# Optimization experiments

Hardware: AMD Instinct MI355X
Metric: run time of the kernel (lower is better)

The kernel has to match this reference:

```python
import jax, jax.numpy as jnp
import numpy as np

LN_EPS = 1e-5
DELTA_FACTOR = 0.01
PATCH_KH, PATCH_KW = 4, 4
SIGMA = 2.0


def layernorm(x, g, b):
    m = jnp.mean(x, axis=-1, keepdims=True)
    v = jnp.var(x, axis=-1, keepdims=True)
    return (x - m) * jax.lax.rsqrt(v + LN_EPS) * g + b


def grid_sample(src, grid):
    # src [B,C,H,W], grid [B,Hg,Wg,2] in [-1,1]; bilinear, align_corners=False, zero padding
    B, C, H, W = src.shape
    Hg, Wg = grid.shape[1], grid.shape[2]
    gx = (grid[..., 0] + 1.0) * (W * 0.5) - 0.5
    gy = (grid[..., 1] + 1.0) * (H * 0.5) - 0.5
    x0 = jnp.floor(gx)
    y0 = jnp.floor(gy)
    wx = gx - x0
    wy = gy - y0
    x0i = x0.astype(jnp.int32)
    y0i = y0.astype(jnp.int32)
    flat = src.reshape(B, C, H * W)

    def tap(xi, yi, w):
        valid = (xi >= 0) & (xi < W) & (yi >= 0) & (yi < H)
        idx = (jnp.clip(yi, 0, H - 1) * W + jnp.clip(xi, 0, W - 1)).reshape(B, -1)
        vals = jax.vmap(lambda f, i: f[:, i])(flat, idx)  # [B,C,Hg*Wg]
        return vals * (w * valid).reshape(B, 1, -1)

    out = (tap(x0i, y0i, (1 - wx) * (1 - wy)) + tap(x0i + 1, y0i, wx * (1 - wy))
           + tap(x0i, y0i + 1, (1 - wx) * wy) + tap(x0i + 1, y0i + 1, wx * wy))
    return out.reshape(B, C, Hg, Wg)


def gaussian_filt(x, k, sigma):
    # depthwise Gaussian blur, NCHW
    C = x.shape[1]
    coords = jnp.arange(k, dtype=x.dtype) - (k - 1) / 2.0
    g2 = jnp.exp(-(coords[:, None] ** 2 + coords[None, :] ** 2) / (2.0 * sigma ** 2))
    g2 = g2 / g2.sum()
    kern = jnp.broadcast_to(g2, (C, 1, k, k))
    p = (k - 1) // 2
    return jax.lax.conv_general_dilated(x, kern, (1, 1), [(p, p), (p, p)],
                                        dimension_numbers=('NCHW', 'OIHW', 'NCHW'),
                                        feature_group_count=C)


def reconstruct_feature(feature, mask, k, sigma):
    if k <= 1:
        return feature
    feature = feature * mask
    out = gaussian_filt(jnp.concatenate([feature, mask], axis=1), k, sigma)
    f_i = out[:, :-1]
    m_i = out[:, -1:]
    f_i = f_i / (m_i + 1e-6)
    f_i = f_i * (m_i > 0)
    return feature + (1 - mask) * f_i


def token2map(x, loc, H, W, k, sigma):
    B, N, C = x.shape
    l = jnp.clip(loc, 0.0, 1.0) * jnp.array([W - 1, H - 1], dtype=loc.dtype)
    l = jnp.round(l).astype(jnp.int32)
    idx = l[..., 0] + l[..., 1] * W + (jnp.arange(B, dtype=jnp.int32) * (H * W))[:, None]
    vals = jnp.concatenate([x, jnp.ones((B, N, 1), x.dtype)], axis=-1).reshape(B * N, C + 1)
    out = jnp.zeros((B * H * W, C + 1), x.dtype).at[idx.reshape(-1)].add(vals)
    out = out.reshape(B, H, W, C + 1).transpose(0, 3, 1, 2)
    feat, mask = out[:, :-1], out[:, -1:]
    feat = feat / (mask + 1e-6)
    mask = (mask > 0).astype(x.dtype)
    feat = feat * mask
    return reconstruct_feature(feat, mask, k, sigma)


def forward(x, loc, src, H, W, kernel_size,
            w_delta, b_delta, norm1_g, norm1_b, conv_w, conv_b,
            norm2_g, norm2_b, fc1_w, fc1_b, fc2_w, fc2_b):
    B, N, _ = loc.shape
    Cs, Hs, Ws = src.shape[1], src.shape[2], src.shape[3]
    delta = (layernorm(x, norm1_g, norm1_b) @ w_delta + b_delta) * DELTA_FACTOR
    loc_extra = jnp.clip(loc + delta, 0.0, 1.0)
    # extract_local_feature: 4x4 sub-pixel patch around each extra location
    xo = (jnp.arange(PATCH_KW, dtype=loc.dtype) - (PATCH_KW - 1) / 2.0) / (Ws - 1)
    yo = (jnp.arange(PATCH_KH, dtype=loc.dtype) - (PATCH_KH - 1) / 2.0) / (Hs - 1)
    off = jnp.stack([jnp.broadcast_to(xo[None, :], (PATCH_KH, PATCH_KW)),
                     jnp.broadcast_to(yo[:, None], (PATCH_KH, PATCH_KW))], axis=-1)
    grid = (loc_extra[:, :, None, None, :] + off[None, None]) * 2.0 - 1.0  # [B,N,kh,kw,2]
    patches = grid_sample(src, grid.reshape(B, N, PATCH_KH * PATCH_KW, 2))  # [B,C,N,kh*kw]
    patches = patches.reshape(B, Cs, N, PATCH_KH, PATCH_KW)
    # local_conv: 4x4 conv stride 4 over a 4x4 patch == single dot product
    extra = jnp.einsum('bcnhw,ochw->bno', patches, conv_w) + conv_b
    extra = layernorm(extra, norm2_g, norm2_b)
    # token2map scatter + gaussian reconstruction, then gather back at loc_extra
    fmap = token2map(x, loc, H, W, kernel_size, SIGMA)
    extra_inter = grid_sample(fmap, (loc_extra * 2.0 - 1.0)[:, None, :, :])  # [B,C,1,N]
    extra_inter = extra_inter[:, :, 0].transpose(0, 2, 1)  # [B,N,C]
    extra = jnp.concatenate([extra_inter, extra], axis=-1)
    h = jax.nn.gelu(extra @ fc1_w + fc1_b, approximate=False)
    extra = h @ fc2_w + fc2_b
    return jnp.concatenate([x, extra], axis=1), jnp.concatenate([loc, loc_extra], axis=1)


def setup_inputs() -> dict:
    key = jax.random.key(0)
    ks = jax.random.split(key, 12)
    B, N, D = 4, 16384, 256
    LD, HID = 64, 4 * D
    inp = {
        'x': jax.random.normal(ks[0], (B, N, D), jnp.float32),
        'loc': jax.random.uniform(ks[1], (B, N, 2), jnp.float32),
        'src': jax.random.normal(ks[2], (B, 3, 512, 512), jnp.float32),
        'pos_embed': jnp.zeros((1,), jnp.float32),
        'H': 128, 'W': 128, 'kernel_size': 3,
        'w_delta': jax.random.normal(ks[3], (D, 2), jnp.float32) * 0.02,
        'b_delta': jnp.zeros((2,), jnp.float32),
        'norm1_g': jnp.ones((D,), jnp.float32),
        'norm1_b': jnp.zeros((D,), jnp.float32),
        'conv_w': jax.random.normal(ks[4], (LD, 3, 4, 4), jnp.float32) * 0.1,
        'conv_b': jnp.zeros((LD,), jnp.float32),
        'norm2_g': jnp.ones((LD,), jnp.float32),
        'norm2_b': jnp.zeros((LD,), jnp.float32),
        'fc1_w': jax.random.normal(ks[5], (D + LD, HID), jnp.float32) * 0.02,
        'fc1_b': jnp.zeros((HID,), jnp.float32),
        'fc2_w': jax.random.normal(ks[6], (HID, D), jnp.float32) * 0.02,
        'fc2_b': jnp.zeros((D,), jnp.float32),
    }
    return inp


def reference(x, loc, src, pos_embed, H, W, kernel_size,
              w_delta, b_delta, norm1_g, norm1_b, conv_w, conv_b,
              norm2_g, norm2_b, fc1_w, fc1_b, fc2_w, fc2_b):
    # pos_embed is accepted by the torch forward but never used
    return forward(x, loc, src, H, W, kernel_size,
                   w_delta, b_delta, norm1_g, norm1_b, conv_w, conv_b,
                   norm2_g, norm2_b, fc1_w, fc1_b, fc2_w, fc2_b)
```

## Files before the change

### kernel.cpp

```cpp
#include <hip/hip_runtime.h>
#include <hip/hip_bf16.h>

#define B_    4
#define N_    16384
#define D_    256
#define LD_   64
#define HID_  1024
#define HW_   128
#define HSRC_ 512
#define CS_   3
#define KIN_  320

typedef __attribute__((ext_vector_type(8))) short bf16x8;
typedef __attribute__((ext_vector_type(4))) float f32x4;

__device__ __forceinline__ float wsum(float v) {
#pragma unroll
  for (int off = 32; off; off >>= 1) v += __shfl_xor(v, off, 64);
  return v;
}

__device__ __forceinline__ unsigned short f2bf(float f) {
  unsigned int u = __float_as_uint(f);
  u = (u + 0x7fffu + ((u >> 16) & 1u)) >> 16;
  return (unsigned short)u;
}

__device__ __forceinline__ void async16(unsigned short* lds, const unsigned short* g) {
  __builtin_amdgcn_global_load_lds(
      (const __attribute__((address_space(1))) unsigned int*)g,
      (__attribute__((address_space(3))) unsigned int*)lds, 16, 0, 0);
}

__global__ __launch_bounds__(256) void k_wconv(const float* __restrict__ fc1w,
                                               const float* __restrict__ fc2w,
                                               unsigned short* __restrict__ bt1,
                                               unsigned short* __restrict__ bt2) {
  int i = blockIdx.x * 256 + threadIdx.x;
  if (i < KIN_ * HID_) {
    int n = i / KIN_, k = i % KIN_;
    bt1[i] = f2bf(fc1w[(size_t)k * HID_ + n]);
  } else {
    int j = i - KIN_ * HID_;
    if (j < D_ * HID_) {
      int n = j / HID_, k = j % HID_;
      bt2[j] = f2bf(fc2w[(size_t)k * D_ + n]);
    }
  }
}

__global__ __launch_bounds__(256) void k_copy_x(const float* __restrict__ x,
                                                float* __restrict__ out0) {
  size_t i = (size_t)blockIdx.x * 256 + threadIdx.x;
  size_t e = i * 4;
  size_t b = e / ((size_t)N_ * D_);
  size_t off = e - b * (size_t)N_ * D_;
  *(float4*)(out0 + b * (size_t)2 * N_ * D_ + off) = *(const float4*)(x + e);
}

__global__ __launch_bounds__(256) void k_delta(const float* __restrict__ x,
                                               const float* __restrict__ loc,
                                               const float* __restrict__ wd,
                                               const float* __restrict__ bd,
                                               const float* __restrict__ g1,
                                               const float* __restrict__ b1,
                                               float* __restrict__ locex,
                                               float* __restrict__ out1) {
  int wv = threadIdx.x >> 6, lane = threadIdx.x & 63;
  int t = blockIdx.x * 4 + wv;
  const float4 xv = *(const float4*)(x + (size_t)t * D_ + lane * 4);
  float m = wsum(xv.x + xv.y + xv.z + xv.w) * (1.0f / D_);
  float d0 = xv.x - m, d1 = xv.y - m, d2 = xv.z - m, d3 = xv.w - m;
  float v = wsum(d0 * d0 + d1 * d1 + d2 * d2 + d3 * d3) * (1.0f / D_);
  float r = rsqrtf(v + 1e-5f);
  const float4 gv = *(const float4*)(g1 + lane * 4);
  const float4 bv = *(const float4*)(b1 + lane * 4);
  float n0 = d0 * r * gv.x + bv.x;
  float n1 = d1 * r * gv.y + bv.y;
  float n2 = d2 * r * gv.z + bv.z;
  float n3 = d3 * r * gv.w + bv.w;
  int i2 = lane * 8;
  float p0 = n0 * wd[i2 + 0] + n1 * wd[i2 + 2] + n2 * wd[i2 + 4] + n3 * wd[i2 + 6];
  float p1 = n0 * wd[i2 + 1] + n1 * wd[i2 + 3] + n2 * wd[i2 + 5] + n3 * wd[i2 + 7];
  p0 = wsum(p0);
  p1 = wsum(p1);
  if (lane == 0) {
    float lx = loc[(size_t)t * 2], ly = loc[(size_t)t * 2 + 1];
    float ex = fminf(fmaxf(lx + (p0 + bd[0]) * 0.01f, 0.0f), 1.0f);
    float ey = fminf(fmaxf(ly + (p1 + bd[1]) * 0.01f, 0.0f), 1.0f);
    locex[(size_t)t * 2] = ex;
    locex[(size_t)t * 2 + 1] = ey;
    int b = t >> 14, n = t & (N_ - 1);
    size_t o1 = (size_t)b * 2 * N_;
    out1[(o1 + n) * 2 + 0] = lx;
    out1[(o1 + n) * 2 + 1] = ly;
    out1[(o1 + N_ + n) * 2 + 0] = ex;
    out1[(o1 + N_ + n) * 2 + 1] = ey;
  }
}

__global__ __launch_bounds__(256) void k_build(const float* __restrict__ loc,
                                               int* __restrict__ head,
                                               int* __restrict__ nxt) {
  int t = blockIdx.x * 256 + threadIdx.x;
  int b = t >> 14;
  float lx = fminf(fmaxf(loc[(size_t)t * 2], 0.0f), 1.0f) * 127.0f;
  float ly = fminf(fmaxf(loc[(size_t)t * 2 + 1], 0.0f), 1.0f) * 127.0f;
  int ix = (int)rintf(lx);
  int iy = (int)rintf(ly);
  int cell = (b << 14) + iy * HW_ + ix;
  nxt[t] = atomicExch(head + cell, t);
}

__global__ __launch_bounds__(256) void k_gather(const float* __restrict__ x,
                                                const int* __restrict__ head,
                                                const int* __restrict__ nxt,
                                                float* __restrict__ featn,
                                                float* __restrict__ cntf) {
  int cell = blockIdx.x;
  int tid = threadIdx.x;
  __shared__ int toks[16];
  __shared__ int scount, snext;
  float acc = 0.0f;
  int total = 0;
  int cur = head[cell];
  while (cur >= 0) {
    if (tid == 0) {
      int c = 0, p = cur;
      while (p >= 0 && c < 16) {
        toks[c++] = p;
        p = nxt[p];
      }
      scount = c;
      snext = p;
    }
    __syncthreads();
    int c = scount;
    for (int i = 0; i < c; ++i) acc += x[(size_t)toks[i] * D_ + tid];
    total += c;
    cur = snext;
    __syncthreads();
  }
  featn[(size_t)cell * D_ + tid] = (total > 0) ? acc / ((float)total + 1e-6f) : 0.0f;
  if (tid == 0) cntf[cell] = (float)total;
}

__global__ __launch_bounds__(256) void k_filter(const float* __restrict__ featn,
                                                const float* __restrict__ cntf,
                                                float* __restrict__ fmap) {
  int pix = blockIdx.x;
  int c = threadIdx.x;
  int b = pix >> 14;
  int p = pix & 16383;
  int y = p >> 7, xc = p & 127;
  float cc = cntf[pix];
  float outv;
  if (cc > 0.0f) {
    outv = featn[(size_t)pix * D_ + c];
  } else {
    float e1 = expf(-0.125f), e2 = expf(-0.25f);
    float sumw = 1.0f + 4.0f * e1 + 4.0f * e2;
    float gf = 0.0f, gm = 0.0f;
#pragma unroll
    for (int dy = -1; dy <= 1; ++dy)
#pragma unroll
      for (int dx = -1; dx <= 1; ++dx) {
        int ny = y + dy, nx = xc + dx;
        if (ny < 0 || ny >= HW_ || nx < 0 || nx >= HW_) continue;
        int q = (b << 14) + ny * HW_ + nx;
        if (cntf[q] > 0.0f) {
          int dd = dy * dy + dx * dx;
          float w = (dd == 0 ? 1.0f : (dd == 1 ? e1 : e2)) / sumw;
          gf += w * featn[(size_t)q * D_ + c];
          gm += w;
        }
      }
    outv = (gm > 0.0f) ? gf / (gm + 1e-6f) : 0.0f;
  }
  fmap[(size_t)pix * D_ + c] = outv;
}

__global__ __launch_bounds__(256) void k_patch(const float* __restrict__ src,
                                               const float* __restrict__ locex,
                                               const float* __restrict__ convw,
                                               const float* __restrict__ convb,
                                               const float* __restrict__ g2,
                                               const float* __restrict__ b2,
                                               unsigned short* __restrict__ ecat) {
  __shared__ float cw[LD_ * 49];
  __shared__ float patch[4][48];
  for (int i = threadIdx.x; i < LD_ * 48; i += 256)
    cw[(i / 48) * 49 + (i % 48)] = convw[i];
  int wv = threadIdx.x >> 6, lane = threadIdx.x & 63;
  int t = blockIdx.x * 4 + wv;
  int b = t >> 14;
  float ex = locex[(size_t)t * 2], ey = locex[(size_t)t * 2 + 1];
  __syncthreads();
  if (lane < 48) {
    int c = lane >> 4, p = lane & 15, py = p >> 2, px = p & 3;
    float u = ex + ((float)px - 1.5f) / 511.0f;
    float vv = ey + ((float)py - 1.5f) / 511.0f;
    float gx = u * 512.0f - 0.5f;
    float gy = vv * 512.0f - 0.5f;
    float fx = floorf(gx), fy = floorf(gy);
    float wx = gx - fx, wy = gy - fy;
    int x0 = (int)fx, y0 = (int)fy;
    const float* plane = src + (size_t)(b * CS_ + c) * (HSRC_ * HSRC_);
    float acc = 0.0f;
#pragma unroll
    for (int ty = 0; ty < 2; ++ty)
#pragma unroll
      for (int tx = 0; tx < 2; ++tx) {
        int xi = x0 + tx, yi = y0 + ty;
        float w = (tx ? wx : 1.0f - wx) * (ty ? wy : 1.0f - wy);
        if (xi >= 0 && xi < HSRC_ && yi >= 0 && yi < HSRC_)
          acc += w * plane[yi * HSRC_ + xi];
      }
    patch[wv][lane] = acc;
  }
  __syncthreads();
  float e = convb[lane];
#pragma unroll
  for (int i = 0; i < 48; ++i) e += patch[wv][i] * cw[lane * 49 + i];
  float m = wsum(e) * (1.0f / 64.0f);
  float d = e - m;
  float v = wsum(d * d) * (1.0f / 64.0f);
  float val = d * rsqrtf(v + 1e-5f) * g2[lane] + b2[lane];
  ecat[(size_t)t * KIN_ + D_ + lane] = f2bf(val);
}

__global__ __launch_bounds__(256) void k_sample(const float* __restrict__ fmap,
                                                const float* __restrict__ locex,
                                                unsigned short* __restrict__ ecat) {
  int wv = threadIdx.x >> 6, lane = threadIdx.x & 63;
  int t = blockIdx.x * 4 + wv;
  int b = t >> 14;
  float gx = locex[(size_t)t * 2] * 128.0f - 0.5f;
  float gy = locex[(size_t)t * 2 + 1] * 128.0f - 0.5f;
  float fx = floorf(gx), fy = floorf(gy);
  float wx = gx - fx, wy = gy - fy;
  int x0 = (int)fx, y0 = (int)fy;
  const float* base = fmap + ((size_t)b << 14) * D_;
  float4 acc = {0.0f, 0.0f, 0.0f, 0.0f};
#pragma unroll
  for (int ty = 0; ty < 2; ++ty)
#pragma unroll
    for (int tx = 0; tx < 2; ++tx) {
      int xi = x0 + tx, yi = y0 + ty;
      float w = (tx ? wx : 1.0f - wx) * (ty ? wy : 1.0f - wy);
      if (xi >= 0 && xi < HW_ && yi >= 0 && yi < HW_) {
        const float4 f = *(const float4*)(base + (size_t)(yi * HW_ + xi) * D_ + lane * 4);
        acc.x += w * f.x;
        acc.y += w * f.y;
        acc.z += w * f.z;
        acc.w += w * f.w;
      }
    }
  ushort4 o;
  o.x = f2bf(acc.x);
  o.y = f2bf(acc.y);
  o.z = f2bf(acc.z);
  o.w = f2bf(acc.w);
  *(ushort4*)(ecat + (size_t)t * KIN_ + lane * 4) = o;
}

template <int GELU>
__global__ __launch_bounds__(256) void k_gemm128(const unsigned short* __restrict__ A,
                                                 const unsigned short* __restrict__ Bt,
                                                 const float* __restrict__ bias, int K,
                                                 int Nn, unsigned short* __restrict__ hout,
                                                 float* __restrict__ out0) {
  __shared__ __align__(16) unsigned short As[128 * 32];
  __shared__ __align__(16) unsigned short Bs[128 * 32];
  int tid = threadIdx.x, wv = tid >> 6, lane = tid & 63;
  int wm = wv & 1, wn = wv >> 1;

  int nt_cnt = gridDim.x;
  int lin = blockIdx.y * nt_cnt + blockIdx.x;
  int xcd = lin & 7;
  int slot = lin >> 3;
  int tile_n = (slot % nt_cnt) * 128;
  int tile_m = ((slot / nt_cnt) * 8 + xcd) * 128;

  f32x4 acc[4][4];
#pragma unroll
  for (int i = 0; i < 4; ++i)
#pragma unroll
    for (int j = 0; j < 4; ++j) acc[i][j] = (f32x4){0.0f, 0.0f, 0.0f, 0.0f};

  int r0 = tid >> 2, c0 = (tid & 3) * 8;
  const unsigned short* ga = A + (size_t)(tile_m + r0) * K + c0;
  const unsigned short* gb = Bt + (size_t)(tile_n + r0) * K + c0;
  size_t rowskip = (size_t)64 * K;
  unsigned short* lA0 = As + tid * 8;
  unsigned short* lA1 = As + 2048 + tid * 8;
  unsigned short* lB0 = Bs + tid * 8;
  unsigned short* lB1 = Bs + 2048 + tid * 8;

  int ar = wm * 64 + (lane & 15);
  int br = wn * 64 + (lane & 15);
  int kk = (lane >> 4) * 8;

  for (int k0 = 0; k0 < K; k0 += 32) {
    async16(lA0, ga);
    async16(lA1, ga + rowskip);
    async16(lB0, gb);
    async16(lB1, gb + rowskip);
    ga += 32;
    gb += 32;
    __syncthreads();
    bf16x8 afr[4], bfr[4];
#pragma unroll
    for (int i = 0; i < 4; ++i) {
      afr[i] = *(const bf16x8*)(As + (ar + i * 16) * 32 + kk);
      bfr[i] = *(const bf16x8*)(Bs + (br + i * 16) * 32 + kk);
    }
#pragma unroll
    for (int mt = 0; mt < 4; ++mt)
#pragma unroll
      for (int nt = 0; nt < 4; ++nt)
        acc[mt][nt] =
            __builtin_amdgcn_mfma_f32_16x16x32_bf16(afr[mt], bfr[nt], acc[mt][nt], 0, 0, 0);
    __syncthreads();
  }

#pragma unroll
  for (int nt = 0; nt < 4; ++nt) {
    int n = tile_n + wn * 64 + nt * 16 + (lane & 15);
    float bv = bias[n];
#pragma unroll
    for (int mt = 0; mt < 4; ++mt) {
      int mbase = tile_m + wm * 64 + mt * 16 + (lane >> 4) * 4;
#pragma unroll
      for (int r = 0; r < 4; ++r) {
        int m = mbase + r;
        float v = acc[mt][nt][r] + bv;
        if (GELU) {
          v = 0.5f * v * (1.0f + erff(v * 0.70710678118654752f));
          hout[(size_t)m * Nn + n] = f2bf(v);
        } else {
          int bb = m >> 14, ntok = m & (N_ - 1);
          out0[((size_t)bb * 2 * N_ + N_ + ntok) * D_ + n] = v;
        }
      }
    }
  }
}

extern "C" void kernel_launch(void* const* d_in, const int* in_sizes, int n_in,
                              void* d_out, int out_size, void* d_ws, size_t ws_size,
                              hipStream_t stream) {
  const float* x = (const float*)d_in[0];
  const float* loc = (const float*)d_in[1];
  const float* src = (const float*)d_in[2];
  const float* wd = (const float*)d_in[7];
  const float* bd = (const float*)d_in[8];
  const float* g1 = (const float*)d_in[9];
  const float* b1 = (const float*)d_in[10];
  const float* cw = (const float*)d_in[11];
  const float* cb = (const float*)d_in[12];
  const float* g2 = (const float*)d_in[13];
  const float* b2 = (const float*)d_in[14];
  const float* fc1w = (const float*)d_in[15];
  const float* fc1b = (const float*)d_in[16];
  const float* fc2w = (const float*)d_in[17];
  const float* fc2b = (const float*)d_in[18];

  float* out0 = (float*)d_out;
  float* out1 = out0 + (size_t)B_ * 2 * N_ * D_;

  char* ws = (char*)d_ws;
  float* featn = (float*)(ws + 0);
  float* fmap = (float*)(ws + 67108864);
  unsigned short* h = (unsigned short*)(ws + 0);
  float* cntf = (float*)(ws + 134217728);
  float* locex = (float*)(ws + 134479872);
  unsigned short* ecat = (unsigned short*)(ws + 135004160);
  unsigned short* bt1 = (unsigned short*)(ws + 176947200);
  unsigned short* bt2 = (unsigned short*)(ws + 177602560);
  int* head = (int*)(ws + 178126848);
  int* nxt = (int*)(ws + 178388992);

  hipMemsetAsync(head, 0xFF, (size_t)262144, stream);

  k_wconv<<<2304, 256, 0, stream>>>(fc1w, fc2w, bt1, bt2);
  k_copy_x<<<16384, 256, 0, stream>>>(x, out0);
  k_delta<<<16384, 256, 0, stream>>>(x, loc, wd, bd, g1, b1, locex, out1);
  k_build<<<256, 256, 0, stream>>>(loc, head, nxt);
  k_gather<<<65536, 256, 0, stream>>>(x, head, nxt, featn, cntf);
  k_filter<<<65536, 256, 0, stream>>>(featn, cntf, fmap);
  k_patch<<<16384, 256, 0, stream>>>(src, locex, cw, cb, g2, b2, ecat);
  k_sample<<<16384, 256, 0, stream>>>(fmap, locex, ecat);
  k_gemm128<1><<<dim3(8, 512), 256, 0, stream>>>(ecat, bt1, fc1b, KIN_, HID_, h, nullptr);
  k_gemm128<0><<<dim3(2, 512), 256, 0, stream>>>(h, bt2, fc2b, HID_, D_, nullptr, out0);
}
```

Before: 592.0 us.

## Fuse copy and bucket build into delta, use bf16 feature maps, retile GEMM

Folds the x copy and the token-to-cell linked-list build into the delta kernel, which removes two launches and a second pass over x. The intermediate feature maps are stored as bf16 to halve the gather, filter and sample traffic, at some cost in precision. The GEMM now uses a K-step of 64 with an XOR-swizzled LDS layout to cut bank conflicts and barrier count. The GELU epilogue switches from erf to a tanh approximation and stages the bf16 output tile through LDS for coalesced 16-byte stores, which also changes numerics slightly.

```diff
diff --git a/kernel.cpp b/kernel.cpp
--- a/kernel.cpp
+++ b/kernel.cpp
@@ -24,6 +24,16 @@
   unsigned int u = __float_as_uint(f);
   u = (u + 0x7fffu + ((u >> 16) & 1u)) >> 16;
   return (unsigned short)u;
+}
+__device__ __forceinline__ float b2f(unsigned short u) {
+  return __uint_as_float(((unsigned int)u) << 16);
+}
+
+__device__ __forceinline__ float gelu_f(float x) {
+  float z = 0.7978845608028654f * (x + 0.044715f * x * x * x);
+  float e = __expf(2.0f * z);
+  float th = 1.0f - 2.0f / (e + 1.0f);
+  return 0.5f * x * (1.0f + th);
 }
 
 __device__ __forceinline__ void async16(unsigned short* lds, const unsigned short* g) {
@@ -49,15 +59,6 @@
   }
 }
 
-__global__ __launch_bounds__(256) void k_copy_x(const float* __restrict__ x,
-                                                float* __restrict__ out0) {
-  size_t i = (size_t)blockIdx.x * 256 + threadIdx.x;
-  size_t e = i * 4;
-  size_t b = e / ((size_t)N_ * D_);
-  size_t off = e - b * (size_t)N_ * D_;
-  *(float4*)(out0 + b * (size_t)2 * N_ * D_ + off) = *(const float4*)(x + e);
-}
-
 __global__ __launch_bounds__(256) void k_delta(const float* __restrict__ x,
                                                const float* __restrict__ loc,
                                                const float* __restrict__ wd,
@@ -65,10 +66,15 @@
                                                const float* __restrict__ g1,
                                                const float* __restrict__ b1,
                                                float* __restrict__ locex,
-                                               float* __restrict__ out1) {
+                                               float* __restrict__ out1,
+                                               float* __restrict__ out0,
+                                               int* __restrict__ head,
+                                               int* __restrict__ nxt) {
   int wv = threadIdx.x >> 6, lane = threadIdx.x & 63;
   int t = blockIdx.x * 4 + wv;
+  int b = t >> 14, n = t & (N_ - 1);
   const float4 xv = *(const float4*)(x + (size_t)t * D_ + lane * 4);
+  *(float4*)(out0 + ((size_t)b * 2 * N_ + n) * D_ + lane * 4) = xv;
   float m = wsum(xv.x + xv.y + xv.z + xv.w) * (1.0f / D_);
   float d0 = xv.x - m, d1 = xv.y - m, d2 = xv.z - m, d3 = xv.w - m;
   float v = wsum(d0 * d0 + d1 * d1 + d2 * d2 + d3 * d3) * (1.0f / D_);
@@ -90,32 +96,24 @@
     float ey = fminf(fmaxf(ly + (p1 + bd[1]) * 0.01f, 0.0f), 1.0f);
     locex[(size_t)t * 2] = ex;
     locex[(size_t)t * 2 + 1] = ey;
-    int b = t >> 14, n = t & (N_ - 1);
     size_t o1 = (size_t)b * 2 * N_;
     out1[(o1 + n) * 2 + 0] = lx;
     out1[(o1 + n) * 2 + 1] = ly;
     out1[(o1 + N_ + n) * 2 + 0] = ex;
     out1[(o1 + N_ + n) * 2 + 1] = ey;
-  }
-}
-
-__global__ __launch_bounds__(256) void k_build(const float* __restrict__ loc,
-                                               int* __restrict__ head,
-                                               int* __restrict__ nxt) {
-  int t = blockIdx.x * 256 + threadIdx.x;
-  int b = t >> 14;
-  float lx = fminf(fmaxf(loc[(size_t)t * 2], 0.0f), 1.0f) * 127.0f;
-  float ly = fminf(fmaxf(loc[(size_t)t * 2 + 1], 0.0f), 1.0f) * 127.0f;
-  int ix = (int)rintf(lx);
-  int iy = (int)rintf(ly);
-  int cell = (b << 14) + iy * HW_ + ix;
-  nxt[t] = atomicExch(head + cell, t);
+    float cx = fminf(fmaxf(lx, 0.0f), 1.0f) * 127.0f;
+    float cy = fminf(fmaxf(ly, 0.0f), 1.0f) * 127.0f;
+    int ix = (int)rintf(cx);
+    int iy = (int)rintf(cy);
+    int cell = (b << 14) + iy * HW_ + ix;
+    nxt[t] = atomicExch(head + cell, t);
+  }
 }
 
 __global__ __launch_bounds__(256) void k_gather(const float* __restrict__ x,
                                                 const int* __restrict__ head,
                                                 const int* __restrict__ nxt,
-                                                float* __restrict__ featn,
+                                                unsigned short* __restrict__ featn,
                                                 float* __restrict__ cntf) {
   int cell = blockIdx.x;
   int tid = threadIdx.x;
@@ -141,20 +139,20 @@
     cur = snext;
     __syncthreads();
   }
-  featn[(size_t)cell * D_ + tid] = (total > 0) ? acc / ((float)total + 1e-6f) : 0.0f;
+  featn[(size_t)cell * D_ + tid] = f2bf((total > 0) ? acc / ((float)total + 1e-6f) : 0.0f);
   if (tid == 0) cntf[cell] = (float)total;
 }
 
-__global__ __launch_bounds__(256) void k_filter(const float* __restrict__ featn,
+__global__ __launch_bounds__(256) void k_filter(const unsigned short* __restrict__ featn,
                                                 const float* __restrict__ cntf,
-                                                float* __restrict__ fmap) {
+                                                unsigned short* __restrict__ fmap) {
   int pix = blockIdx.x;
   int c = threadIdx.x;
   int b = pix >> 14;
   int p = pix & 16383;
   int y = p >> 7, xc = p & 127;
   float cc = cntf[pix];
-  float outv;
+  unsigned short outv;
   if (cc > 0.0f) {
     outv = featn[(size_t)pix * D_ + c];
   } else {
@@ -171,11 +169,11 @@
         if (cntf[q] > 0.0f) {
           int dd = dy * dy + dx * dx;
           float w = (dd == 0 ? 1.0f : (dd == 1 ? e1 : e2)) / sumw;
-          gf += w * featn[(size_t)q * D_ + c];
+          gf += w * b2f(featn[(size_t)q * D_ + c]);
           gm += w;
         }
       }
-    outv = (gm > 0.0f) ? gf / (gm + 1e-6f) : 0.0f;
+    outv = f2bf((gm > 0.0f) ? gf / (gm + 1e-6f) : 0.0f);
   }
   fmap[(size_t)pix * D_ + c] = outv;
 }
@@ -229,7 +227,7 @@
   ecat[(size_t)t * KIN_ + D_ + lane] = f2bf(val);
 }
 
-__global__ __launch_bounds__(256) void k_sample(const float* __restrict__ fmap,
+__global__ __launch_bounds__(256) void k_sample(const unsigned short* __restrict__ fmap,
                                                 const float* __restrict__ locex,
                                                 unsigned short* __restrict__ ecat) {
   int wv = threadIdx.x >> 6, lane = threadIdx.x & 63;
@@ -240,7 +238,7 @@
   float fx = floorf(gx), fy = floorf(gy);
   float wx = gx - fx, wy = gy - fy;
   int x0 = (int)fx, y0 = (int)fy;
-  const float* base = fmap + ((size_t)b << 14) * D_;
+  const unsigned short* base = fmap + (((size_t)b << 14)) * D_;
   float4 acc = {0.0f, 0.0f, 0.0f, 0.0f};
 #pragma unroll
   for (int ty = 0; ty < 2; ++ty)
@@ -249,11 +247,11 @@
       int xi = x0 + tx, yi = y0 + ty;
       float w = (tx ? wx : 1.0f - wx) * (ty ? wy : 1.0f - wy);
       if (xi >= 0 && xi < HW_ && yi >= 0 && yi < HW_) {
-        const float4 f = *(const float4*)(base + (size_t)(yi * HW_ + xi) * D_ + lane * 4);
-        acc.x += w * f.x;
-        acc.y += w * f.y;
-        acc.z += w * f.z;
-        acc.w += w * f.w;
+        ushort4 f = *(const ushort4*)(base + (size_t)(yi * HW_ + xi) * D_ + lane * 4);
+        acc.x += w * b2f(f.x);
+        acc.y += w * b2f(f.y);
+        acc.z += w * b2f(f.z);
+        acc.w += w * b2f(f.w);
       }
     }
   ushort4 o;
@@ -270,8 +268,9 @@
                                                  const float* __restrict__ bias, int K,
                                                  int Nn, unsigned short* __restrict__ hout,
                                                  float* __restrict__ out0) {
-  __shared__ __align__(16) unsigned short As[128 * 32];
-  __shared__ __align__(16) unsigned short Bs[128 * 32];
+  __shared__ __align__(16) unsigned short sh[16384];
+  unsigned short* As = sh;
+  unsigned short* Bs = sh + 8192;
   int tid = threadIdx.x, wv = tid >> 6, lane = tid & 63;
   int wm = wv & 1, wn = wv >> 1;
 
@@ -288,57 +287,78 @@
 #pragma unroll
     for (int j = 0; j < 4; ++j) acc[i][j] = (f32x4){0.0f, 0.0f, 0.0f, 0.0f};
 
-  int r0 = tid >> 2, c0 = (tid & 3) * 8;
-  const unsigned short* ga = A + (size_t)(tile_m + r0) * K + c0;
-  const unsigned short* gb = Bt + (size_t)(tile_n + r0) * K + c0;
-  size_t rowskip = (size_t)64 * K;
-  unsigned short* lA0 = As + tid * 8;
-  unsigned short* lA1 = As + 2048 + tid * 8;
-  unsigned short* lB0 = Bs + tid * 8;
-  unsigned short* lB1 = Bs + 2048 + tid * 8;
+  int srow = tid >> 3;
+  int schunk = (tid & 7) ^ (srow & 7);
+  const unsigned short* ga = A + (size_t)(tile_m + srow) * K + schunk * 8;
+  const unsigned short* gb = Bt + (size_t)(tile_n + srow) * K + schunk * 8;
+  size_t skip = (size_t)32 * K;
+  int lofs = tid * 8;
 
   int ar = wm * 64 + (lane & 15);
   int br = wn * 64 + (lane & 15);
-  int kk = (lane >> 4) * 8;
-
-  for (int k0 = 0; k0 < K; k0 += 32) {
-    async16(lA0, ga);
-    async16(lA1, ga + rowskip);
-    async16(lB0, gb);
-    async16(lB1, gb + rowskip);
-    ga += 32;
-    gb += 32;
+  int ksel = lane >> 4;
+  int sw = lane & 7;
+
+  for (int k0 = 0; k0 < K; k0 += 64) {
+#pragma unroll
+    for (int c = 0; c < 4; ++c) async16(As + c * 2048 + lofs, ga + c * skip);
+#pragma unroll
+    for (int c = 0; c < 4; ++c) async16(Bs + c * 2048 + lofs, gb + c * skip);
+    ga += 64;
+    gb += 64;
     __syncthreads();
-    bf16x8 afr[4], bfr[4];
-#pragma unroll
-    for (int i = 0; i < 4; ++i) {
-      afr[i] = *(const bf16x8*)(As + (ar + i * 16) * 32 + kk);
-      bfr[i] = *(const bf16x8*)(Bs + (br + i * 16) * 32 + kk);
-    }
-#pragma unroll
-    for (int mt = 0; mt < 4; ++mt)
-#pragma unroll
-      for (int nt = 0; nt < 4; ++nt)
-        acc[mt][nt] =
-            __builtin_amdgcn_mfma_f32_16x16x32_bf16(afr[mt], bfr[nt], acc[mt][nt], 0, 0, 0);
+#pragma unroll
+    for (int j = 0; j < 2; ++j) {
+      bf16x8 afr[4], bfr[4];
+      int ca = ((j * 4 + ksel) ^ sw) * 8;
+#pragma unroll
+      for (int i = 0; i < 4; ++i) {
+        afr[i] = *(const bf16x8*)(As + (ar + i * 16) * 64 + ca);
+        bfr[i] = *(const bf16x8*)(Bs + (br + i * 16) * 64 + ca);
+      }
+#pragma unroll
+      for (int mt = 0; mt < 4; ++mt)
+#pragma unroll
+        for (int nt = 0; nt < 4; ++nt)
+          acc[mt][nt] =
+              __builtin_amdgcn_mfma_f32_16x16x32_bf16(afr[mt], bfr[nt], acc[mt][nt], 0, 0, 0);
+    }
     __syncthreads();
   }
 
-#pragma unroll
-  for (int nt = 0; nt < 4; ++nt) {
-    int n = tile_n + wn * 64 + nt * 16 + (lane & 15);
-    float bv = bias[n];
-#pragma unroll
-    for (int mt = 0; mt < 4; ++mt) {
-      int mbase = tile_m + wm * 64 + mt * 16 + (lane >> 4) * 4;
-#pragma unroll
-      for (int r = 0; r < 4; ++r) {
-        int m = mbase + r;
-        float v = acc[mt][nt][r] + bv;
-        if (GELU) {
-          v = 0.5f * v * (1.0f + erff(v * 0.70710678118654752f));
-          hout[(size_t)m * Nn + n] = f2bf(v);
-        } else {
+  if (GELU) {
+#pragma unroll
+    for (int nt = 0; nt < 4; ++nt) {
+      int nl = wn * 64 + nt * 16 + (lane & 15);
+      float bv = bias[tile_n + nl];
+#pragma unroll
+      for (int mt = 0; mt < 4; ++mt) {
+        int ml = wm * 64 + mt * 16 + (lane >> 4) * 4;
+#pragma unroll
+        for (int r = 0; r < 4; ++r)
+          sh[(ml + r) * 128 + nl] = f2bf(gelu_f(acc[mt][nt][r] + bv));
+      }
+    }
+    __syncthreads();
+#pragma unroll
+    for (int it = 0; it < 8; ++it) {
+      int idx = it * 256 + tid;
+      int row = idx >> 4, ch = (idx & 15) * 8;
+      *(uint4*)(hout + (size_t)(tile_m + row) * Nn + tile_n + ch) =
+          *(const uint4*)(sh + row * 128 + ch);
+    }
+  } else {
+#pragma unroll
+    for (int nt = 0; nt < 4; ++nt) {
+      int n = tile_n + wn * 64 + nt * 16 + (lane & 15);
+      float bv = bias[n];
+#pragma unroll
+      for (int mt = 0; mt < 4; ++mt) {
+        int mbase = tile_m + wm * 64 + mt * 16 + (lane >> 4) * 4;
+#pragma unroll
+        for (int r = 0; r < 4; ++r) {
+          int m = mbase + r;
+          float v = acc[mt][nt][r] + bv;
           int bb = m >> 14, ntok = m & (N_ - 1);
           out0[((size_t)bb * 2 * N_ + N_ + ntok) * D_ + n] = v;
         }
@@ -370,23 +390,21 @@
   float* out1 = out0 + (size_t)B_ * 2 * N_ * D_;
 
   char* ws = (char*)d_ws;
-  float* featn = (float*)(ws + 0);
-  float* fmap = (float*)(ws + 67108864);
+  unsigned short* featn = (unsigned short*)(ws + 0);
+  unsigned short* fmap = (unsigned short*)(ws + 33554432);
   unsigned short* h = (unsigned short*)(ws + 0);
-  float* cntf = (float*)(ws + 134217728);
-  float* locex = (float*)(ws + 134479872);
-  unsigned short* ecat = (unsigned short*)(ws + 135004160);
-  unsigned short* bt1 = (unsigned short*)(ws + 176947200);
-  unsigned short* bt2 = (unsigned short*)(ws + 177602560);
+  unsigned short* ecat = (unsigned short*)(ws + 134217728);
+  unsigned short* bt1 = (unsigned short*)(ws + 176160768);
+  unsigned short* bt2 = (unsigned short*)(ws + 176816128);
+  float* cntf = (float*)(ws + 177340416);
+  float* locex = (float*)(ws + 177602560);
   int* head = (int*)(ws + 178126848);
   int* nxt = (int*)(ws + 178388992);
 
   hipMemsetAsync(head, 0xFF, (size_t)262144, stream);
 
   k_wconv<<<2304, 256, 0, stream>>>(fc1w, fc2w, bt1, bt2);
-  k_copy_x<<<16384, 256, 0, stream>>>(x, out0);
-  k_delta<<<16384, 256, 0, stream>>>(x, loc, wd, bd, g1, b1, locex, out1);
-  k_build<<<256, 256, 0, stream>>>(loc, head, nxt);
+  k_delta<<<16384, 256, 0, stream>>>(x, loc, wd, bd, g1, b1, locex, out1, out0, head, nxt);
   k_gather<<<65536, 256, 0, stream>>>(x, head, nxt, featn, cntf);
   k_filter<<<65536, 256, 0, stream>>>(featn, cntf, fmap);
   k_patch<<<16384, 256, 0, stream>>>(src, locex, cw, cb, g2, b2, ecat);
```

Result: faster. 563.0 us (-4.9%).
